# Kernel optimization log

Measured on AMD Instinct MI355X. Metric: run time of the kernel, lower is better.

Reference implementation:

```python
import jax, jax.numpy as jnp
import numpy as np

AUX_COEF = 0.001
Z_COEF = 0.001


def setup_inputs() -> dict:
    key = jax.random.key(0)
    ks = jax.random.split(key, 6)
    B, S, H, E, F = 4, 2048, 1024, 8, 2048
    scale_h = 1.0 / np.sqrt(H)
    scale_f = 1.0 / np.sqrt(F)
    return {
        "hidden_states": jax.random.normal(ks[0], (B, S, H), jnp.float32),
        "router_w": jax.random.normal(ks[1], (E, H), jnp.float32) * scale_h,
        "w1": jax.random.normal(ks[2], (E, H, F), jnp.float32) * scale_h,
        "b1": jax.random.normal(ks[3], (E, F), jnp.float32) * 0.01,
        "w2": jax.random.normal(ks[4], (E, F, H), jnp.float32) * scale_f,
        "b2": jax.random.normal(ks[5], (E, H), jnp.float32) * 0.01,
        "num_experts_per_tok": 2,
    }


def reference(hidden_states, router_w, w1, b1, w2, b2, num_experts_per_tok):
    B, S, H = hidden_states.shape
    E = router_w.shape[0]
    x = hidden_states.reshape(-1, H)  # [T, H]

    # Router
    logits = jnp.einsum('th,eh->te', x, router_w)  # [T, E]
    logp = jax.nn.log_softmax(logits, axis=-1)
    probs = jnp.exp(logp)

    # Top-k routing mask (note: original code does NOT weight by top_k probs)
    _, top_idx = jax.lax.top_k(probs, num_experts_per_tok)  # [T, K]
    mask = jax.nn.one_hot(top_idx, E, dtype=x.dtype).sum(axis=-2)  # [T, E] 0/1

    # Losses: KL(probs || uniform) with torch kl_div(batchmean over dim0=B) + z-loss
    ideal = 1.0 / E
    aux_loss = (ideal * (jnp.log(jnp.float32(ideal)) - logp)).sum() / B * AUX_COEF
    z_loss = jnp.mean(jnp.square(logits)) * Z_COEF
    router_loss = aux_loss + z_loss

    # Dense grouped expert MLP, combined with 0/1 routing mask
    h = jnp.einsum('th,ehf->tef', x, w1) + b1  # [T, E, F]
    h = jax.nn.silu(h)
    y = jnp.einsum('tef,efh->teh', h, w2) + b2  # [T, E, H]
    out = jnp.einsum('teh,te->th', y, mask).reshape(B, S, H)
    return out, router_loss
```

## Files before the change

### kernel.cpp

```cpp
#include <hip/hip_runtime.h>
#include <stdint.h>

#define T_TOK 8192
#define H_DIM 1024
#define E_NUM 8
#define F_DIM 2048
#define BATCH 4
#define AUX_COEF 0.001f
#define Z_COEF 0.001f

#define NBLK_TOK 32

#define GBM 256
#define GBN 256
#define GBK 64
#define MT_CAP 16

typedef __bf16 bf16x8 __attribute__((ext_vector_type(8)));
typedef float f32x4 __attribute__((ext_vector_type(4)));

__device__ __forceinline__ unsigned short f2bf(float f) {
    union { float f; uint32_t u; } v; v.f = f;
    uint32_t u = v.u;
    return (unsigned short)((u + 0x7FFFu + ((u >> 16) & 1u)) >> 16);
}
__device__ __forceinline__ float bf2f(unsigned short u) {
    union { uint32_t u; float f; } v; v.u = ((uint32_t)u) << 16; return v.f;
}

__device__ __forceinline__ void gl_lds16(const void* g, void* l) {
    __builtin_amdgcn_global_load_lds((const __attribute__((address_space(1))) uint32_t*)g,
                                     (__attribute__((address_space(3))) uint32_t*)l, 16, 0, 0);
}

__global__ void transpose_conv_kernel(const float* __restrict__ in, unsigned short* __restrict__ out,
                                      int R, int C) {
    __shared__ float tile[32][33];
    int e = blockIdx.z;
    const float* ine = in + (size_t)e * R * C;
    unsigned short* oute = out + (size_t)e * R * C;
    int tx = threadIdx.x & 31, ty = threadIdx.x >> 5;
    int c0 = blockIdx.x * 32, r0 = blockIdx.y * 32;
#pragma unroll
    for (int i = 0; i < 4; i++) {
        int r = r0 + ty + i * 8;
        tile[ty + i * 8][tx] = ine[(size_t)r * C + c0 + tx];
    }
    __syncthreads();
#pragma unroll
    for (int i = 0; i < 4; i++) {
        int c = c0 + ty + i * 8;
        oute[(size_t)c * R + r0 + tx] = f2bf(tile[tx][ty + i * 8]);
    }
}

__global__ void router_kernel(const float* __restrict__ x, const float* __restrict__ rw,
                              unsigned short* __restrict__ xb,
                              int* __restrict__ top2, float2* __restrict__ loss_part) {
    int wave = threadIdx.x >> 6;
    int lane = threadIdx.x & 63;
    int t = blockIdx.x * 4 + wave;
    const float4* xr = (const float4*)(x + (size_t)t * H_DIM);
    float4 xv[4];
#pragma unroll
    for (int k = 0; k < 4; k++) xv[k] = xr[lane + 64 * k];
    uint2* xo = (uint2*)(xb + (size_t)t * H_DIM);
#pragma unroll
    for (int k = 0; k < 4; k++) {
        uint2 o;
        o.x = (uint32_t)f2bf(xv[k].x) | ((uint32_t)f2bf(xv[k].y) << 16);
        o.y = (uint32_t)f2bf(xv[k].z) | ((uint32_t)f2bf(xv[k].w) << 16);
        xo[lane + 64 * k] = o;
    }
    float acc[E_NUM];
#pragma unroll
    for (int e = 0; e < E_NUM; e++) {
        const float4* rr = (const float4*)(rw + e * H_DIM);
        float s = 0.f;
#pragma unroll
        for (int k = 0; k < 4; k++) {
            float4 r = rr[lane + 64 * k];
            s += xv[k].x * r.x + xv[k].y * r.y + xv[k].z * r.z + xv[k].w * r.w;
        }
        acc[e] = s;
    }
#pragma unroll
    for (int e = 0; e < E_NUM; e++) {
        float v = acc[e];
#pragma unroll
        for (int off = 32; off; off >>= 1) v += __shfl_xor(v, off);
        acc[e] = v;
    }
    __shared__ float red[8];
    if (lane == 0) {
        float mx = acc[0];
#pragma unroll
        for (int e = 1; e < E_NUM; e++) mx = fmaxf(mx, acc[e]);
        float s = 0.f;
#pragma unroll
        for (int e = 0; e < E_NUM; e++) s += expf(acc[e] - mx);
        float lse = mx + logf(s);
        float slogp = 0.f, ssq = 0.f;
#pragma unroll
        for (int e = 0; e < E_NUM; e++) { slogp += acc[e] - lse; ssq += acc[e] * acc[e]; }
        int i1 = 0; float m1 = acc[0];
#pragma unroll
        for (int e = 1; e < E_NUM; e++) if (acc[e] > m1) { m1 = acc[e]; i1 = e; }
        int i2 = -1; float m2 = -1e30f;
#pragma unroll
        for (int e = 0; e < E_NUM; e++) if (e != i1 && acc[e] > m2) { m2 = acc[e]; i2 = e; }
        top2[t] = i1 | (i2 << 8);
        red[wave] = slogp;
        red[4 + wave] = ssq;
    }
    __syncthreads();
    if (threadIdx.x == 0) {
        float2 p;
        p.x = red[0] + red[1] + red[2] + red[3];
        p.y = red[4] + red[5] + red[6] + red[7];
        loss_part[blockIdx.x] = p;
    }
}

__global__ void hist_kernel(const int* __restrict__ top2, int* __restrict__ blockcounts) {
    __shared__ int cnt[E_NUM];
    if (threadIdx.x < E_NUM) cnt[threadIdx.x] = 0;
    __syncthreads();
    int t = blockIdx.x * 256 + threadIdx.x;
    int v = top2[t];
    atomicAdd(&cnt[v & 255], 1);
    atomicAdd(&cnt[v >> 8], 1);
    __syncthreads();
    if (threadIdx.x < E_NUM) blockcounts[blockIdx.x * E_NUM + threadIdx.x] = cnt[threadIdx.x];
}

__global__ void scan_kernel(const int* __restrict__ blockcounts, const float2* __restrict__ loss_part,
                            int* __restrict__ counts, int* __restrict__ basep, int* __restrict__ offs,
                            float* __restrict__ loss_out) {
    __shared__ float redx[4], redy[4];
    int tid = threadIdx.x;
    float sx = 0.f, sy = 0.f;
    for (int i = tid; i < T_TOK / 4; i += 256) {
        float2 p = loss_part[i];
        sx += p.x; sy += p.y;
    }
#pragma unroll
    for (int off = 32; off; off >>= 1) { sx += __shfl_xor(sx, off); sy += __shfl_xor(sy, off); }
    if ((tid & 63) == 0) { redx[tid >> 6] = sx; redy[tid >> 6] = sy; }
    __syncthreads();
    if (tid == 0) {
        float slogp = redx[0] + redx[1] + redx[2] + redx[3];
        float ssq = redy[0] + redy[1] + redy[2] + redy[3];
        float ideal = 1.0f / E_NUM;
        float aux = ideal * ((float)T_TOK * E_NUM * logf(ideal) - slogp) / BATCH * AUX_COEF;
        float z = ssq / ((float)T_TOK * E_NUM) * Z_COEF;
        loss_out[0] = aux + z;
    }
    if (tid < E_NUM) {
        int s = 0;
        for (int b = 0; b < NBLK_TOK; b++) s += blockcounts[b * E_NUM + tid];
        counts[tid] = s;
    }
    __syncthreads();
    if (tid == 0) {
        int s = 0;
        for (int e = 0; e < E_NUM; e++) { basep[e] = s; s += counts[e]; }
    }
    __syncthreads();
    if (tid < E_NUM) {
        int o = basep[tid];
        for (int b = 0; b < NBLK_TOK; b++) { offs[b * E_NUM + tid] = o; o += blockcounts[b * E_NUM + tid]; }
    }
}

__global__ void scatter_kernel(const int* __restrict__ top2, const int* __restrict__ offs,
                               int* __restrict__ rowlist, int* __restrict__ posv) {
    __shared__ int cur[E_NUM];
    if (threadIdx.x < E_NUM) cur[threadIdx.x] = 0;
    __syncthreads();
    int t = blockIdx.x * 256 + threadIdx.x;
    int v = top2[t];
    int e0 = v & 255, e1 = v >> 8;
    int r0 = atomicAdd(&cur[e0], 1);
    int r1 = atomicAdd(&cur[e1], 1);
    int p0 = offs[blockIdx.x * E_NUM + e0] + r0;
    int p1 = offs[blockIdx.x * E_NUM + e1] + r1;
    rowlist[p0] = t;
    rowlist[p1] = t;
    posv[t] = p0 | (p1 << 16);
}

__global__ void combine_kernel(const int* __restrict__ top2, const int* __restrict__ posv,
                               const unsigned short* __restrict__ ybuf, const float* __restrict__ b2,
                               float* __restrict__ out) {
    int t = blockIdx.x;
    int v = top2[t];
    int p = posv[t];
    int e0 = v & 255, e1 = v >> 8;
    int p0 = p & 0xffff, p1 = (p >> 16) & 0xffff;
    int i = threadIdx.x;
    const ushort4* y0 = (const ushort4*)(ybuf + (size_t)p0 * H_DIM);
    const ushort4* y1 = (const ushort4*)(ybuf + (size_t)p1 * H_DIM);
    const float4* q0 = (const float4*)(b2 + (size_t)e0 * H_DIM);
    const float4* q1 = (const float4*)(b2 + (size_t)e1 * H_DIM);
    ushort4 a = y0[i], b = y1[i];
    float4 c0 = q0[i], c1 = q1[i];
    float4 o;
    o.x = bf2f(a.x) + bf2f(b.x) + c0.x + c1.x;
    o.y = bf2f(a.y) + bf2f(b.y) + c0.y + c1.y;
    o.z = bf2f(a.z) + bf2f(b.z) + c0.z + c1.z;
    o.w = bf2f(a.w) + bf2f(b.w) + c0.w + c1.w;
    ((float4*)(out + (size_t)t * H_DIM))[i] = o;
}

template<int KD, int NTILES_N, bool IS_G1>
__global__ __launch_bounds__(512, 2)
void gemm8p(const unsigned short* __restrict__ A,
            const unsigned short* __restrict__ Bt,
            const float* __restrict__ bias_p,
            const int* __restrict__ rowlist,
            const int* __restrict__ basep,
            const int* __restrict__ counts,
            unsigned short* __restrict__ Out)
{
    constexpr int ND = NTILES_N * GBN;
    constexpr int NKT = KD / GBK;
    static_assert(NKT >= 4, "pipeline needs >=4 K-tiles");

    int bid = blockIdx.x;
    int e = bid & 7;
    int q = bid >> 3;
    int nt = q % NTILES_N;
    int mt = q / NTILES_N;
    int n_e = counts[e];
    if (mt * GBM >= n_e) return;
    int base_e = basep[e];

    __shared__ __attribute__((aligned(16))) unsigned char lds[2][65536];

    int tid = threadIdx.x;
    int wv = tid >> 6, lane = tid & 63;

    int srow = tid >> 3;
    int gc = (tid & 7) ^ (srow & 7);
    const unsigned short* aS[4];
    const unsigned short* bS[4];
#pragma unroll
    for (int i = 0; i < 4; i++) {
        int r = srow + i * 64;
        size_t ra;
        if (IS_G1) {
            int rr = min(mt * GBM + r, n_e - 1);
            ra = (size_t)rowlist[base_e + rr];
        } else {
            ra = (size_t)(base_e + min(mt * GBM + r, n_e - 1));
        }
        aS[i] = A + ra * KD + gc * 8;
        bS[i] = Bt + ((size_t)e * ND + nt * GBN + r) * KD + gc * 8;
    }

    auto stageA = [&](int buf, int h, int t) {
        char* d = (char*)lds + buf * 65536 + h * 16384 + wv * 1024;
        gl_lds16(aS[h * 2 + 0] + t * GBK, d);
        gl_lds16(aS[h * 2 + 1] + t * GBK, d + 8192);
    };
    auto stageB = [&](int buf, int h, int t) {
        char* d = (char*)lds + buf * 65536 + 32768 + h * 16384 + wv * 1024;
        gl_lds16(bS[h * 2 + 0] + t * GBK, d);
        gl_lds16(bS[h * 2 + 1] + t * GBK, d + 8192);
    };

    int mlane = lane & 15, quad = lane >> 4;
    int wr = (wv >> 2) * 128;
    int wc = (wv & 3) * 64;
    int xk0 = (quad * 16) ^ ((mlane & 7) << 4);
    int xk1 = (64 + quad * 16) ^ ((mlane & 7) << 4);
    int aRow = (wr + mlane) * 128;
    int bRow = 32768 + (wc + mlane) * 128;

    f32x4 acc[8][4] = {};
    bf16x8 a03[4][2], a47[4][2], b01[2][2], b23[2][2];

    stageA(0, 0, 0); stageA(0, 1, 0); stageB(0, 0, 0); stageB(0, 1, 0);
    if (NKT > 1) { stageB(1, 0, 1); stageA(1, 0, 1); }
    asm volatile("s_waitcnt vmcnt(4)" ::: "memory");
    __builtin_amdgcn_s_barrier();

    for (int t = 0; t < NKT; ++t) {
        const char* Ab = (const char*)lds + (t & 1) * 65536;
        int nb = (t + 1) & 1;

#pragma unroll
        for (int mi = 0; mi < 4; mi++) {
            a03[mi][0] = *(const bf16x8*)(Ab + aRow + mi * 2048 + xk0);
            a03[mi][1] = *(const bf16x8*)(Ab + aRow + mi * 2048 + xk1);
        }
#pragma unroll
        for (int ni = 0; ni < 2; ni++) {
            b01[ni][0] = *(const bf16x8*)(Ab + bRow + ni * 2048 + xk0);
            b01[ni][1] = *(const bf16x8*)(Ab + bRow + ni * 2048 + xk1);
        }
        if (t + 1 < NKT) stageB(nb, 1, t + 1);
        __builtin_amdgcn_s_barrier();
        asm volatile("s_waitcnt lgkmcnt(0)" ::: "memory");
        __builtin_amdgcn_sched_barrier(0);
        __builtin_amdgcn_s_setprio(1);
#pragma unroll
        for (int ks = 0; ks < 2; ks++)
#pragma unroll
            for (int mi = 0; mi < 4; mi++)
#pragma unroll
                for (int ni = 0; ni < 2; ni++)
                    acc[mi][ni] = __builtin_amdgcn_mfma_f32_16x16x32_bf16(a03[mi][ks], b01[ni][ks], acc[mi][ni], 0, 0, 0);
        __builtin_amdgcn_s_setprio(0);
        __builtin_amdgcn_s_barrier();

#pragma unroll
        for (int ni = 0; ni < 2; ni++) {
            b23[ni][0] = *(const bf16x8*)(Ab + bRow + (ni + 2) * 2048 + xk0);
            b23[ni][1] = *(const bf16x8*)(Ab + bRow + (ni + 2) * 2048 + xk1);
        }
        if (t + 1 < NKT) stageA(nb, 1, t + 1);
        __builtin_amdgcn_s_barrier();
        asm volatile("s_waitcnt lgkmcnt(0)" ::: "memory");
        __builtin_amdgcn_sched_barrier(0);
        __builtin_amdgcn_s_setprio(1);
#pragma unroll
        for (int ks = 0; ks < 2; ks++)
#pragma unroll
            for (int mi = 0; mi < 4; mi++)
#pragma unroll
                for (int ni = 0; ni < 2; ni++)
                    acc[mi][ni + 2] = __builtin_amdgcn_mfma_f32_16x16x32_bf16(a03[mi][ks], b23[ni][ks], acc[mi][ni + 2], 0, 0, 0);
        __builtin_amdgcn_s_setprio(0);
        __builtin_amdgcn_s_barrier();

#pragma unroll
        for (int mi = 0; mi < 4; mi++) {
            a47[mi][0] = *(const bf16x8*)(Ab + aRow + (mi + 4) * 2048 + xk0);
            a47[mi][1] = *(const bf16x8*)(Ab + aRow + (mi + 4) * 2048 + xk1);
        }
        if (t + 2 < NKT) stageB(t & 1, 0, t + 2);
        __builtin_amdgcn_s_barrier();
        asm volatile("s_waitcnt lgkmcnt(0)" ::: "memory");
        __builtin_amdgcn_sched_barrier(0);
        __builtin_amdgcn_s_setprio(1);
#pragma unroll
        for (int ks = 0; ks < 2; ks++)
#pragma unroll
            for (int mi = 0; mi < 4; mi++)
#pragma unroll
                for (int ni = 0; ni < 2; ni++)
                    acc[mi + 4][ni] = __builtin_amdgcn_mfma_f32_16x16x32_bf16(a47[mi][ks], b01[ni][ks], acc[mi + 4][ni], 0, 0, 0);
        __builtin_amdgcn_s_setprio(0);
        __builtin_amdgcn_s_barrier();

        if (t + 2 < NKT) stageA(t & 1, 0, t + 2);
        __builtin_amdgcn_s_barrier();
        __builtin_amdgcn_sched_barrier(0);
        __builtin_amdgcn_s_setprio(1);
#pragma unroll
        for (int ks = 0; ks < 2; ks++)
#pragma unroll
            for (int mi = 0; mi < 4; mi++)
#pragma unroll
                for (int ni = 0; ni < 2; ni++)
                    acc[mi + 4][ni + 2] = __builtin_amdgcn_mfma_f32_16x16x32_bf16(a47[mi][ks], b23[ni][ks], acc[mi + 4][ni + 2], 0, 0, 0);
        __builtin_amdgcn_s_setprio(0);
        if (t + 2 < NKT) {
            asm volatile("s_waitcnt vmcnt(4)" ::: "memory");
        } else {
            asm volatile("s_waitcnt vmcnt(0)" ::: "memory");
        }
        __builtin_amdgcn_s_barrier();
    }

    float bias[4];
#pragma unroll
    for (int ni = 0; ni < 4; ni++) {
        if (IS_G1) bias[ni] = bias_p[(size_t)e * ND + nt * GBN + wc + ni * 16 + mlane];
        else bias[ni] = 0.f;
    }
#pragma unroll
    for (int mi = 0; mi < 8; mi++) {
        int mbase = mt * GBM + wr + mi * 16 + quad * 4;
#pragma unroll
        for (int r = 0; r < 4; r++) {
            int m = mbase + r;
            if (m < n_e) {
                unsigned short* orow = Out + (size_t)(base_e + m) * ND + nt * GBN + wc + mlane;
#pragma unroll
                for (int ni = 0; ni < 4; ni++) {
                    float c = acc[mi][ni][r] + bias[ni];
                    if (IS_G1) c = c / (1.f + __expf(-c));
                    orow[ni * 16] = f2bf(c);
                }
            }
        }
    }
}

extern "C" void kernel_launch(void* const* d_in, const int* in_sizes, int n_in,
                              void* d_out, int out_size, void* d_ws, size_t ws_size,
                              hipStream_t stream) {
    const float* x = (const float*)d_in[0];
    const float* rw = (const float*)d_in[1];
    const float* w1 = (const float*)d_in[2];
    const float* b1 = (const float*)d_in[3];
    const float* w2 = (const float*)d_in[4];
    const float* b2 = (const float*)d_in[5];
    float* out = (float*)d_out;

    char* ws = (char*)d_ws;
    int* counts      = (int*)(ws + 0);
    int* basep       = (int*)(ws + 64);
    int* blockcounts = (int*)(ws + 128);
    int* offs        = (int*)(ws + 2048);
    float2* loss_part = (float2*)(ws + 4096);
    int* top2        = (int*)(ws + 32768);
    int* rowlist     = (int*)(ws + 65536);
    int* posv        = (int*)(ws + 131072);
    unsigned short* xb  = (unsigned short*)(ws + 163840);
    unsigned short* w1t = (unsigned short*)(ws + 163840 + 16777216ULL);
    unsigned short* w2t = (unsigned short*)(ws + 163840 + 16777216ULL + 33554432ULL);
    unsigned short* h1  = (unsigned short*)(ws + 163840 + 16777216ULL + 2ULL * 33554432ULL);
    unsigned short* ybuf = w1t;

    transpose_conv_kernel<<<dim3(64, 32, 8), 256, 0, stream>>>(w1, w1t, H_DIM, F_DIM);
    transpose_conv_kernel<<<dim3(32, 64, 8), 256, 0, stream>>>(w2, w2t, F_DIM, H_DIM);
    router_kernel<<<T_TOK / 4, 256, 0, stream>>>(x, rw, xb, top2, loss_part);
    hist_kernel<<<NBLK_TOK, 256, 0, stream>>>(top2, blockcounts);
    scan_kernel<<<1, 256, 0, stream>>>(blockcounts, loss_part, counts, basep, offs,
                                       out + (size_t)T_TOK * H_DIM);
    scatter_kernel<<<NBLK_TOK, 256, 0, stream>>>(top2, offs, rowlist, posv);
    gemm8p<H_DIM, F_DIM / GBN, true><<<8 * MT_CAP * (F_DIM / GBN), 512, 0, stream>>>(
        xb, w1t, b1, rowlist, basep, counts, h1);
    gemm8p<F_DIM, H_DIM / GBN, false><<<8 * MT_CAP * (H_DIM / GBN), 512, 0, stream>>>(
        h1, w2t, nullptr, rowlist, basep, counts, ybuf);
    combine_kernel<<<T_TOK, 256, 0, stream>>>(top2, posv, ybuf, b2, out);
}
```

Before: 449.5 us.

## Overlap LDS fragment reads with MFMA via double-buffered B registers

Restructures the grouped-GEMM main loop so LDS reads for the next K-tile's fragments are issued before each MFMA quadrant and only waited on afterwards. Previously every quadrant waited on its own reads first. B fragments are double-buffered in registers and the loop is unrolled by two to swap buffers. Two full K-tiles are prefetched up front and the vmcnt waits are retuned to match. This hides LDS latency behind matrix-core work, at the cost of more VGPR pressure under launch_bounds(512,2) and a new requirement that the K-tile count be even.

```diff
diff --git a/kernel.cpp b/kernel.cpp
--- a/kernel.cpp
+++ b/kernel.cpp
@@ -225,7 +225,7 @@
 {
     constexpr int ND = NTILES_N * GBN;
     constexpr int NKT = KD / GBK;
-    static_assert(NKT >= 4, "pipeline needs >=4 K-tiles");
+    static_assert(NKT >= 4 && (NKT & 1) == 0, "pipeline needs even NKT >= 4");
 
     int bid = blockIdx.x;
     int e = bid & 7;
@@ -279,100 +279,98 @@
     int bRow = 32768 + (wc + mlane) * 128;
 
     f32x4 acc[8][4] = {};
-    bf16x8 a03[4][2], a47[4][2], b01[2][2], b23[2][2];
-
-    stageA(0, 0, 0); stageA(0, 1, 0); stageB(0, 0, 0); stageB(0, 1, 0);
-    if (NKT > 1) { stageB(1, 0, 1); stageA(1, 0, 1); }
+    bf16x8 a03[4][2], a47[4][2];
+    bf16x8 b01A[2][2], b01B[2][2], b23A[2][2], b23B[2][2];
+
+    auto read_a = [&](const char* buf, int mbase, bf16x8 (&dst)[4][2]) {
+#pragma unroll
+        for (int mi = 0; mi < 4; mi++) {
+            dst[mi][0] = *(const bf16x8*)(buf + aRow + (mbase + mi) * 2048 + xk0);
+            dst[mi][1] = *(const bf16x8*)(buf + aRow + (mbase + mi) * 2048 + xk1);
+        }
+    };
+    auto read_b = [&](const char* buf, int nbase, bf16x8 (&dst)[2][2]) {
+#pragma unroll
+        for (int ni = 0; ni < 2; ni++) {
+            dst[ni][0] = *(const bf16x8*)(buf + bRow + (nbase + ni) * 2048 + xk0);
+            dst[ni][1] = *(const bf16x8*)(buf + bRow + (nbase + ni) * 2048 + xk1);
+        }
+    };
+    auto mfma_q = [&](int am, int bn, bf16x8 (&Af)[4][2], bf16x8 (&Bf)[2][2]) {
+        __builtin_amdgcn_s_setprio(1);
+#pragma unroll
+        for (int ks = 0; ks < 2; ks++)
+#pragma unroll
+            for (int mi = 0; mi < 4; mi++)
+#pragma unroll
+                for (int ni = 0; ni < 2; ni++)
+                    acc[am + mi][bn + ni] =
+                        __builtin_amdgcn_mfma_f32_16x16x32_bf16(Af[mi][ks], Bf[ni][ks], acc[am + mi][bn + ni], 0, 0, 0);
+        __builtin_amdgcn_s_setprio(0);
+        __builtin_amdgcn_sched_barrier(0);
+    };
+
+    stageB(0, 0, 0); stageB(0, 1, 0); stageA(0, 0, 0); stageA(0, 1, 0);
+    stageB(1, 0, 1); stageB(1, 1, 1); stageA(1, 0, 1); stageA(1, 1, 1);
+    asm volatile("s_waitcnt vmcnt(8)" ::: "memory");
+    __builtin_amdgcn_s_barrier();
+    read_a((const char*)lds, 0, a03);
+    read_b((const char*)lds, 0, b01A);
+    read_b((const char*)lds, 2, b23A);
+    asm volatile("s_waitcnt lgkmcnt(0)" ::: "memory");
     asm volatile("s_waitcnt vmcnt(4)" ::: "memory");
     __builtin_amdgcn_s_barrier();
 
-    for (int t = 0; t < NKT; ++t) {
-        const char* Ab = (const char*)lds + (t & 1) * 65536;
-        int nb = (t + 1) & 1;
-
-#pragma unroll
-        for (int mi = 0; mi < 4; mi++) {
-            a03[mi][0] = *(const bf16x8*)(Ab + aRow + mi * 2048 + xk0);
-            a03[mi][1] = *(const bf16x8*)(Ab + aRow + mi * 2048 + xk1);
-        }
-#pragma unroll
-        for (int ni = 0; ni < 2; ni++) {
-            b01[ni][0] = *(const bf16x8*)(Ab + bRow + ni * 2048 + xk0);
-            b01[ni][1] = *(const bf16x8*)(Ab + bRow + ni * 2048 + xk1);
-        }
-        if (t + 1 < NKT) stageB(nb, 1, t + 1);
-        __builtin_amdgcn_s_barrier();
+    auto tile = [&](int t, int cbi,
+                    bf16x8 (&b01_cur)[2][2], bf16x8 (&b01_nxt)[2][2],
+                    bf16x8 (&b23_cur)[2][2], bf16x8 (&b23_nxt)[2][2]) {
+        const char* Nb = (const char*)lds + (cbi ^ 1) * 65536;
+        bool hv1 = (t + 1 < NKT), hv2 = (t + 2 < NKT);
+
+        if (hv1) read_b(Nb, 2, b23_nxt);
+        if (hv2) stageB(cbi, 0, t + 2);
+        __builtin_amdgcn_sched_barrier(0);
+        __builtin_amdgcn_s_barrier();
+        __builtin_amdgcn_sched_barrier(0);
+        mfma_q(0, 0, a03, b01_cur);
         asm volatile("s_waitcnt lgkmcnt(0)" ::: "memory");
-        __builtin_amdgcn_sched_barrier(0);
-        __builtin_amdgcn_s_setprio(1);
-#pragma unroll
-        for (int ks = 0; ks < 2; ks++)
-#pragma unroll
-            for (int mi = 0; mi < 4; mi++)
-#pragma unroll
-                for (int ni = 0; ni < 2; ni++)
-                    acc[mi][ni] = __builtin_amdgcn_mfma_f32_16x16x32_bf16(a03[mi][ks], b01[ni][ks], acc[mi][ni], 0, 0, 0);
-        __builtin_amdgcn_s_setprio(0);
-        __builtin_amdgcn_s_barrier();
-
-#pragma unroll
-        for (int ni = 0; ni < 2; ni++) {
-            b23[ni][0] = *(const bf16x8*)(Ab + bRow + (ni + 2) * 2048 + xk0);
-            b23[ni][1] = *(const bf16x8*)(Ab + bRow + (ni + 2) * 2048 + xk1);
-        }
-        if (t + 1 < NKT) stageA(nb, 1, t + 1);
-        __builtin_amdgcn_s_barrier();
+        __builtin_amdgcn_s_barrier();
+
+        read_a((const char*)lds + cbi * 65536, 4, a47);
+        if (hv2) stageB(cbi, 1, t + 2);
+        __builtin_amdgcn_sched_barrier(0);
+        __builtin_amdgcn_s_barrier();
+        __builtin_amdgcn_sched_barrier(0);
+        mfma_q(0, 2, a03, b23_cur);
         asm volatile("s_waitcnt lgkmcnt(0)" ::: "memory");
-        __builtin_amdgcn_sched_barrier(0);
-        __builtin_amdgcn_s_setprio(1);
-#pragma unroll
-        for (int ks = 0; ks < 2; ks++)
-#pragma unroll
-            for (int mi = 0; mi < 4; mi++)
-#pragma unroll
-                for (int ni = 0; ni < 2; ni++)
-                    acc[mi][ni + 2] = __builtin_amdgcn_mfma_f32_16x16x32_bf16(a03[mi][ks], b23[ni][ks], acc[mi][ni + 2], 0, 0, 0);
-        __builtin_amdgcn_s_setprio(0);
-        __builtin_amdgcn_s_barrier();
-
-#pragma unroll
-        for (int mi = 0; mi < 4; mi++) {
-            a47[mi][0] = *(const bf16x8*)(Ab + aRow + (mi + 4) * 2048 + xk0);
-            a47[mi][1] = *(const bf16x8*)(Ab + aRow + (mi + 4) * 2048 + xk1);
-        }
-        if (t + 2 < NKT) stageB(t & 1, 0, t + 2);
-        __builtin_amdgcn_s_barrier();
+        __builtin_amdgcn_s_barrier();
+
+        if (hv1) read_b(Nb, 0, b01_nxt);
+        if (hv2) stageA(cbi, 0, t + 2);
+        __builtin_amdgcn_sched_barrier(0);
+        __builtin_amdgcn_s_barrier();
+        __builtin_amdgcn_sched_barrier(0);
+        mfma_q(4, 0, a47, b01_cur);
         asm volatile("s_waitcnt lgkmcnt(0)" ::: "memory");
-        __builtin_amdgcn_sched_barrier(0);
-        __builtin_amdgcn_s_setprio(1);
-#pragma unroll
-        for (int ks = 0; ks < 2; ks++)
-#pragma unroll
-            for (int mi = 0; mi < 4; mi++)
-#pragma unroll
-                for (int ni = 0; ni < 2; ni++)
-                    acc[mi + 4][ni] = __builtin_amdgcn_mfma_f32_16x16x32_bf16(a47[mi][ks], b01[ni][ks], acc[mi + 4][ni], 0, 0, 0);
-        __builtin_amdgcn_s_setprio(0);
-        __builtin_amdgcn_s_barrier();
-
-        if (t + 2 < NKT) stageA(t & 1, 0, t + 2);
-        __builtin_amdgcn_s_barrier();
-        __builtin_amdgcn_sched_barrier(0);
-        __builtin_amdgcn_s_setprio(1);
-#pragma unroll
-        for (int ks = 0; ks < 2; ks++)
-#pragma unroll
-            for (int mi = 0; mi < 4; mi++)
-#pragma unroll
-                for (int ni = 0; ni < 2; ni++)
-                    acc[mi + 4][ni + 2] = __builtin_amdgcn_mfma_f32_16x16x32_bf16(a47[mi][ks], b23[ni][ks], acc[mi + 4][ni + 2], 0, 0, 0);
-        __builtin_amdgcn_s_setprio(0);
-        if (t + 2 < NKT) {
-            asm volatile("s_waitcnt vmcnt(4)" ::: "memory");
-        } else {
-            asm volatile("s_waitcnt vmcnt(0)" ::: "memory");
-        }
-        __builtin_amdgcn_s_barrier();
+        if (hv2) { asm volatile("s_waitcnt vmcnt(6)" ::: "memory"); }
+        else     { asm volatile("s_waitcnt vmcnt(0)" ::: "memory"); }
+        __builtin_amdgcn_s_barrier();
+
+        if (hv1) read_a(Nb, 0, a03);
+        if (hv2) stageA(cbi, 1, t + 2);
+        __builtin_amdgcn_sched_barrier(0);
+        __builtin_amdgcn_s_barrier();
+        __builtin_amdgcn_sched_barrier(0);
+        mfma_q(4, 2, a47, b23_cur);
+        asm volatile("s_waitcnt lgkmcnt(0)" ::: "memory");
+        if (hv2) { asm volatile("s_waitcnt vmcnt(4)" ::: "memory"); }
+        else     { asm volatile("s_waitcnt vmcnt(0)" ::: "memory"); }
+        __builtin_amdgcn_s_barrier();
+    };
+
+    for (int tb = 0; tb < NKT; tb += 2) {
+        tile(tb,     0, b01A, b01B, b23A, b23B);
+        tile(tb + 1, 1, b01B, b01A, b23B, b23A);
     }
 
     float bias[4];
```

Measured after the change: 1.224 ms. 2.72x slower.
